# Kernel optimization log

Hardware: AMD Instinct MI355X
Metric: run time of the kernel (lower is better)

The kernel has to match this reference:

```python
import jax, jax.numpy as jnp
import numpy as np


def setup_inputs() -> dict:
    key = jax.random.key(0)
    ks = jax.random.split(key, 8)
    B, N, D = 8, 2048, 128
    s = 1.0 / float(np.sqrt(D))
    node = jax.random.normal(ks[0], (B, N, D), dtype=jnp.float32)
    node_mask = jax.random.randint(ks[1], (B, N), 0, 2, dtype=jnp.int32)
    punctuation_graph = jax.random.randint(ks[2], (B, N, N), 0, 2, dtype=jnp.int32)
    w_nw = jax.random.uniform(ks[3], (1, D), jnp.float32, -s, s)
    b_nw = jax.random.uniform(ks[4], (1,), jnp.float32, -s, s)
    w_self = jax.random.uniform(ks[5], (D, D), jnp.float32, -s, s)
    b_self = jax.random.uniform(ks[6], (D,), jnp.float32, -s, s)
    w_punct = jax.random.uniform(ks[7], (D, D), jnp.float32, -s, s)
    return {"node": node, "node_mask": node_mask, "punctuation_graph": punctuation_graph,
            "w_nw": w_nw, "b_nw": b_nw, "w_self": w_self, "b_self": b_self,
            "w_punct": w_punct, "iteration_steps": 2}


def reference(node, node_mask, punctuation_graph, w_nw, b_nw, w_self, b_self, w_punct, iteration_steps):
    B, N, D = node.shape
    # dd_graph = mask outer product with zeroed diagonal; graph = dd_graph * punctuation_graph
    eye = jnp.eye(N, dtype=punctuation_graph.dtype)
    dd = node_mask[:, None, :] * node_mask[:, :, None] * (1 - eye)[None, :, :]  # [B,N,N]
    graph = dd * punctuation_graph  # [B,N,N] int, binary
    nbr_num = graph.sum(-1)  # [B,N]
    # replace_masked_values(nbr_num, nbr_num>=1, 1): nodes with no neighbors get denom 1
    nbr_f = jnp.where(nbr_num >= 1, nbr_num.astype(node.dtype), jnp.asarray(1.0, node.dtype))
    gmask = graph > 0
    weights = []
    x = node
    for _ in range(iteration_steps):  # small fixed step count
        dw = jax.nn.sigmoid(jnp.einsum('bnd,od->bno', x, w_nw) + b_nw)[..., 0]  # [B,N]
        weights.append(dw)
        self_info = jnp.einsum('bnd,ed->bne', x, w_self) + b_self  # [B,N,D]
        info_p = jnp.einsum('bnd,ed->bne', x, w_punct)  # [B,N,D]
        # node_weight[b,i,j] = dw[b,j] where graph[b,i,j] else 0
        nw = jnp.where(gmask, dw[:, None, :], jnp.asarray(0.0, x.dtype))  # [B,N,N]
        agg = jnp.einsum('bnm,bmd->bnd', nw, info_p) / nbr_f[..., None]
        x = jax.nn.relu(self_info + agg)
    all_weight = jnp.stack(weights, axis=1)  # [B, steps, N]
    return x, all_weight
```

## Files before the change

kernel.cpp:

```cpp
#include <hip/hip_runtime.h>
#include <hip/hip_bf16.h>

#define BB 8
#define NN 2048
#define DD 128

typedef __attribute__((ext_vector_type(8))) __bf16 bf16x8;
typedef __attribute__((ext_vector_type(4))) float f32x4;
typedef __attribute__((ext_vector_type(4))) int   i32x4;

static __device__ __forceinline__ unsigned short f2bf(float f) {
    union { float f; unsigned u; } v; v.f = f;
    unsigned r = (v.u + 0x7FFFu + ((v.u >> 16) & 1u)) >> 16;
    return (unsigned short)r;
}
static __device__ __forceinline__ float bf2f(unsigned short b) {
    union { unsigned u; float f; } v; v.u = ((unsigned)b) << 16;
    return v.f;
}

__global__ __launch_bounds__(256) void kernPW(
    const int* __restrict__ punct, const int* __restrict__ mask,
    const float* __restrict__ node, const float* __restrict__ w_self,
    const float* __restrict__ w_punct,
    unsigned* __restrict__ pk, float* __restrict__ scale_g, float* __restrict__ pdm_g,
    unsigned short* __restrict__ xb, unsigned short* __restrict__ wsb,
    unsigned short* __restrict__ wpb)
{
    const int t = threadIdx.x;
    const int bid = blockIdx.x;

    if (bid < 4096) {
        const int wave = t >> 6, lane = t & 63;
        const int row_g = bid * 4 + wave;
        const int b = row_g >> 11;
        const int i = row_g & (NN - 1);

        const int* prow = punct + (size_t)row_g * NN;
        const int* mrow = mask + (size_t)b * NN;

        unsigned pk0 = 0, pk1 = 0;
        int acc = 0;
        #pragma unroll 4
        for (int w = 0; w < 32; ++w) {
            const int col = w * 64 + lane;
            const int p = prow[col];
            const int m = mrow[col];
            const int pred = (p & m) & 1;
            unsigned long long bal = __ballot(pred);
            if (lane == w) { pk0 = (unsigned)bal; pk1 = (unsigned)(bal >> 32); }
            acc += pred + ((col == i ? pred : 0) << 16);
        }
        #pragma unroll
        for (int o = 32; o > 0; o >>= 1) acc += __shfl_xor(acc, o, 64);

        if (lane < 32) {
            uint2 w2; w2.x = pk0; w2.y = pk1;
            *(uint2*)(pk + (size_t)row_g * 64 + 2 * lane) = w2;
        }
        if (lane == 0) {
            const int nall = acc & 0xFFFF;
            const int pdm  = acc >> 16;
            const int mi   = mrow[i];
            const int nbr  = nall - pdm;
            scale_g[row_g] = mi ? 1.f / (float)(nbr < 1 ? 1 : nbr) : 0.f;
            pdm_g[row_g]   = (float)pdm;
        }
        return;
    }

    const int cb = bid - 4096;
    const float* src; unsigned short* dst; size_t base;
    if (cb < 1024)      { src = node;    dst = xb;  base = (size_t)cb * 2048; }
    else if (cb < 1032) { src = w_self;  dst = wsb; base = (size_t)(cb - 1024) * 2048; }
    else                { src = w_punct; dst = wpb; base = (size_t)(cb - 1032) * 2048; }
    const size_t i0 = base + (size_t)t * 8;
    f32x4 a = *(const f32x4*)(src + i0);
    f32x4 c = *(const f32x4*)(src + i0 + 4);
    unsigned q0 = f2bf(a.x) | ((unsigned)f2bf(a.y) << 16);
    unsigned q1 = f2bf(a.z) | ((unsigned)f2bf(a.w) << 16);
    unsigned q2 = f2bf(c.x) | ((unsigned)f2bf(c.y) << 16);
    unsigned q3 = f2bf(c.z) | ((unsigned)f2bf(c.w) << 16);
    i32x4 pw = {(int)q0, (int)q1, (int)q2, (int)q3};
    *(i32x4*)(dst + i0) = pw;
}

__global__ __launch_bounds__(256) void kernB(
    const unsigned short* __restrict__ xb,
    const float* __restrict__ xf,
    const unsigned short* __restrict__ wsb,
    const unsigned short* __restrict__ wpb,
    const float* __restrict__ w_nw, const float* __restrict__ b_nw,
    const float* __restrict__ b_self,
    float* __restrict__ si_out,
    unsigned short* __restrict__ yne_out,
    unsigned short* __restrict__ yT_out,
    float* __restrict__ aw_out)
{
    __shared__ float dw_l[32];
    __shared__ unsigned short ytl[128 * 40];

    const int t  = threadIdx.x;
    const int n0 = blockIdx.x * 32;
    const int b  = n0 >> 11;
    const int nb = n0 & (NN - 1);
    const int wave = t >> 6, lane = t & 63;
    const int quad = lane >> 4, l16 = lane & 15;

    {
        const int row = wave * 8 + (lane >> 3);
        const int seg = (lane & 7) * 16;
        const float* xr = xf + (size_t)(n0 + row) * DD + seg;
        const float* wr = w_nw + seg;
        f32x4 a0 = *(const f32x4*)xr,       a1 = *(const f32x4*)(xr + 4);
        f32x4 a2 = *(const f32x4*)(xr + 8), a3 = *(const f32x4*)(xr + 12);
        f32x4 w0 = *(const f32x4*)wr,       w1 = *(const f32x4*)(wr + 4);
        f32x4 w2 = *(const f32x4*)(wr + 8), w3 = *(const f32x4*)(wr + 12);
        float s = a0.x*w0.x + a0.y*w0.y + a0.z*w0.z + a0.w*w0.w
                + a1.x*w1.x + a1.y*w1.y + a1.z*w1.z + a1.w*w1.w
                + a2.x*w2.x + a2.y*w2.y + a2.z*w2.z + a2.w*w2.w
                + a3.x*w3.x + a3.y*w3.y + a3.z*w3.z + a3.w*w3.w;
        s += __shfl_xor(s, 1, 64);
        s += __shfl_xor(s, 2, 64);
        s += __shfl_xor(s, 4, 64);
        if ((lane & 7) == 0) {
            float dv = 1.f / (1.f + __expf(-(s + b_nw[0])));
            dw_l[row] = dv;
            aw_out[(size_t)b * 2 * NN + nb + row] = dv;
        }
    }

    f32x4 accs[2][2] = {}, accp[2][2] = {};
    const unsigned short* xrow = xb + (size_t)n0 * DD;
    #pragma unroll
    for (int kk = 0; kk < 4; ++kk) {
        const int k0 = kk * 32 + quad * 8;
        bf16x8 af[2], bs[2], bp[2];
        #pragma unroll
        for (int mt = 0; mt < 2; ++mt)
            af[mt] = *(const bf16x8*)(xrow + (size_t)(mt * 16 + l16) * DD + k0);
        #pragma unroll
        for (int nt = 0; nt < 2; ++nt) {
            const int e = wave * 32 + nt * 16 + l16;
            bs[nt] = *(const bf16x8*)(wsb + (size_t)e * DD + k0);
            bp[nt] = *(const bf16x8*)(wpb + (size_t)e * DD + k0);
        }
        #pragma unroll
        for (int mt = 0; mt < 2; ++mt)
            #pragma unroll
            for (int nt = 0; nt < 2; ++nt) {
                accs[mt][nt] = __builtin_amdgcn_mfma_f32_16x16x32_bf16(af[mt], bs[nt], accs[mt][nt], 0, 0, 0);
                accp[mt][nt] = __builtin_amdgcn_mfma_f32_16x16x32_bf16(af[mt], bp[nt], accp[mt][nt], 0, 0, 0);
            }
    }

    __syncthreads();
    #pragma unroll
    for (int mt = 0; mt < 2; ++mt) {
        #pragma unroll
        for (int nt = 0; nt < 2; ++nt) {
            const int e = wave * 32 + nt * 16 + l16;
            const float bsv = b_self[e];
            #pragma unroll
            for (int r = 0; r < 4; ++r) {
                const int nl = mt * 16 + quad * 4 + r;
                const size_t idx = (size_t)(n0 + nl) * DD + e;
                si_out[idx] = accs[mt][nt][r] + bsv;
                const float yv = dw_l[nl] * accp[mt][nt][r];
                const unsigned short ub = f2bf(yv);
                yne_out[idx] = ub;
                ytl[e * 40 + nl] = ub;
            }
        }
    }
    __syncthreads();
    {
        const int e = t >> 1, half = t & 1;
        const i32x4* src = (const i32x4*)&ytl[e * 40 + half * 16];
        i32x4 v0 = src[0], v1 = src[1];
        i32x4* dst = (i32x4*)(yT_out + (size_t)(b * DD + e) * NN + nb + half * 16);
        dst[0] = v0; dst[1] = v1;
    }
}

__global__ __launch_bounds__(256) void kernC(
    const unsigned* __restrict__ pk,
    const float* __restrict__ scale_g, const float* __restrict__ pdm_g,
    const unsigned short* __restrict__ yT,
    const float* __restrict__ si,
    const unsigned short* __restrict__ yne,
    float* __restrict__ x_out,
    unsigned short* __restrict__ xb_out)
{
    __shared__ unsigned pPk[32 * 68];
    __shared__ float scale_l[32];
    __shared__ float pdm_l[32];

    const int t  = threadIdx.x;
    const int b  = blockIdx.x & 7;
    const int i0 = (blockIdx.x >> 3) * 32;
    const size_t rg0 = (size_t)b * NN + i0;

    #pragma unroll
    for (int r = 0; r < 2; ++r) {
        const int u   = r * 256 + t;
        const int row = u >> 4;
        const int wq  = (u & 15) * 4;
        i32x4 v = *(const i32x4*)(pk + (rg0 + row) * 64 + wq);
        *(i32x4*)&pPk[row * 68 + wq] = v;
    }
    if (t < 32) {
        scale_l[t] = scale_g[rg0 + t];
        pdm_l[t]   = pdm_g[rg0 + t];
    }
    __syncthreads();

    const int wn = t >> 6, lane = t & 63;
    const int quad = lane >> 4, l16 = lane & 15;
    const unsigned short* yTb = yT + (size_t)b * DD * NN;

    f32x4 acc[2][2] = {};

    #pragma unroll 4
    for (int kk = 0; kk < 64; ++kk) {
        bf16x8 bfr[2];
        #pragma unroll
        for (int nt = 0; nt < 2; ++nt) {
            const int e = wn * 32 + nt * 16 + l16;
            bfr[nt] = *(const bf16x8*)(yTb + (size_t)e * NN + kk * 32 + quad * 8);
        }
        bf16x8 af[2];
        #pragma unroll
        for (int mt = 0; mt < 2; ++mt) {
            const unsigned w = pPk[(mt * 16 + l16) * 68 + kk];
            const unsigned by = (w >> (quad * 8)) & 0xFFu;
            i32x4 ex;
            ex.x = ((by &   1u) ? 0x3F80 : 0) | ((by &   2u) ? 0x3F800000 : 0);
            ex.y = ((by &   4u) ? 0x3F80 : 0) | ((by &   8u) ? 0x3F800000 : 0);
            ex.z = ((by &  16u) ? 0x3F80 : 0) | ((by &  32u) ? 0x3F800000 : 0);
            ex.w = ((by &  64u) ? 0x3F80 : 0) | ((by & 128u) ? 0x3F800000 : 0);
            union { i32x4 i; bf16x8 h; } cv; cv.i = ex;
            af[mt] = cv.h;
        }
        #pragma unroll
        for (int mt = 0; mt < 2; ++mt)
            #pragma unroll
            for (int nt = 0; nt < 2; ++nt)
                acc[mt][nt] = __builtin_amdgcn_mfma_f32_16x16x32_bf16(af[mt], bfr[nt], acc[mt][nt], 0, 0, 0);
    }

    #pragma unroll
    for (int mt = 0; mt < 2; ++mt) {
        #pragma unroll
        for (int nt = 0; nt < 2; ++nt) {
            const int e = wn * 32 + nt * 16 + l16;
            #pragma unroll
            for (int r = 0; r < 4; ++r) {
                const int row = mt * 16 + quad * 4 + r;
                const size_t idx = (rg0 + row) * DD + e;
                const float yv = bf2f(yne[idx]);
                float v = si[idx] + scale_l[row] * (acc[mt][nt][r] - pdm_l[row] * yv);
                v = fmaxf(v, 0.f);
                x_out[idx]  = v;
                xb_out[idx] = f2bf(v);
            }
        }
    }
}

extern "C" void kernel_launch(void* const* d_in, const int* in_sizes, int n_in,
                              void* d_out, int out_size, void* d_ws, size_t ws_size,
                              hipStream_t stream) {
    const float* node   = (const float*)d_in[0];
    const int*   mask   = (const int*)  d_in[1];
    const int*   punct  = (const int*)  d_in[2];
    const float* w_nw   = (const float*)d_in[3];
    const float* b_nw   = (const float*)d_in[4];
    const float* w_self = (const float*)d_in[5];
    const float* b_self = (const float*)d_in[6];
    const float* w_punct= (const float*)d_in[7];

    float* xout = (float*)d_out;
    float* aw   = xout + (size_t)BB * NN * DD;

    char* w = (char*)d_ws;
    float*          si   = (float*)w;
    unsigned short* yne  = (unsigned short*)(w + (8u  << 20));
    unsigned short* yT   = (unsigned short*)(w + (12u << 20));
    unsigned*       pk   = (unsigned*)(w + (16u << 20));
    float*          scl  = (float*)(w + (20u << 20));
    float*          pdm  = (float*)(w + (20u << 20) + (64u << 10));
    unsigned short* xb   = (unsigned short*)(w + (21u << 20));
    unsigned short* wsb  = (unsigned short*)(w + (25u << 20));
    unsigned short* wpb  = (unsigned short*)(w + (25u << 20) + (32u << 10));

    dim3 blk(256);
    kernPW<<<dim3(5136), blk, 0, stream>>>(punct, mask, node, w_self, w_punct,
                                           pk, scl, pdm, xb, wsb, wpb);
    kernB<<<dim3(512), blk, 0, stream>>>(xb, node, wsb, wpb, w_nw, b_nw, b_self,
                                         si, yne, yT, aw);
    kernC<<<dim3(512), blk, 0, stream>>>(pk, scl, pdm, yT, si, yne, xout, xb);
    kernB<<<dim3(512), blk, 0, stream>>>(xb, xout, wsb, wpb, w_nw, b_nw, b_self,
                                         si, yne, yT, aw + NN);
    kernC<<<dim3(512), blk, 0, stream>>>(pk, scl, pdm, yT, si, yne, xout, xb);
}
```

Measured before the change: 304.3 us.

## Fuse both iteration steps into one persistent kernel with grid barrier

Replaces the four per-step launches with a single persistent kernel of 256 blocks of 512 threads. Each block keeps its weights, packed graph rows and 64-row activation tile in shared memory across both steps and synchronises the grid with an atomic-counter barrier. This removes launch gaps and the global round trips for self_info, y and the bf16 activations. The bf16 conversion of node and weights is folded into the kernel, and yT is double-buffered per step. The costs are lower parallelism (256 blocks), large shared memory use, and reliance on all blocks being co-resident for the spin barrier to avoid deadlock.

Result: slower. 347.1 us (+14.0%).

```diff
diff --git a/kernel.cpp b/kernel.cpp
--- a/kernel.cpp
+++ b/kernel.cpp
@@ -18,253 +18,287 @@
     union { unsigned u; float f; } v; v.u = ((unsigned)b) << 16;
     return v.f;
 }
-
-__global__ __launch_bounds__(256) void kernPW(
-    const int* __restrict__ punct, const int* __restrict__ mask,
-    const float* __restrict__ node, const float* __restrict__ w_self,
-    const float* __restrict__ w_punct,
-    unsigned* __restrict__ pk, float* __restrict__ scale_g, float* __restrict__ pdm_g,
-    unsigned short* __restrict__ xb, unsigned short* __restrict__ wsb,
-    unsigned short* __restrict__ wpb)
-{
-    const int t = threadIdx.x;
-    const int bid = blockIdx.x;
-
-    if (bid < 4096) {
-        const int wave = t >> 6, lane = t & 63;
-        const int row_g = bid * 4 + wave;
-        const int b = row_g >> 11;
-        const int i = row_g & (NN - 1);
-
-        const int* prow = punct + (size_t)row_g * NN;
-        const int* mrow = mask + (size_t)b * NN;
-
-        unsigned pk0 = 0, pk1 = 0;
-        int acc = 0;
-        #pragma unroll 4
-        for (int w = 0; w < 32; ++w) {
-            const int col = w * 64 + lane;
-            const int p = prow[col];
-            const int m = mrow[col];
-            const int pred = (p & m) & 1;
-            unsigned long long bal = __ballot(pred);
-            if (lane == w) { pk0 = (unsigned)bal; pk1 = (unsigned)(bal >> 32); }
-            acc += pred + ((col == i ? pred : 0) << 16);
-        }
-        #pragma unroll
-        for (int o = 32; o > 0; o >>= 1) acc += __shfl_xor(acc, o, 64);
-
-        if (lane < 32) {
-            uint2 w2; w2.x = pk0; w2.y = pk1;
-            *(uint2*)(pk + (size_t)row_g * 64 + 2 * lane) = w2;
-        }
-        if (lane == 0) {
-            const int nall = acc & 0xFFFF;
-            const int pdm  = acc >> 16;
-            const int mi   = mrow[i];
-            const int nbr  = nall - pdm;
-            scale_g[row_g] = mi ? 1.f / (float)(nbr < 1 ? 1 : nbr) : 0.f;
-            pdm_g[row_g]   = (float)pdm;
-        }
-        return;
-    }
-
-    const int cb = bid - 4096;
-    const float* src; unsigned short* dst; size_t base;
-    if (cb < 1024)      { src = node;    dst = xb;  base = (size_t)cb * 2048; }
-    else if (cb < 1032) { src = w_self;  dst = wsb; base = (size_t)(cb - 1024) * 2048; }
-    else                { src = w_punct; dst = wpb; base = (size_t)(cb - 1032) * 2048; }
-    const size_t i0 = base + (size_t)t * 8;
-    f32x4 a = *(const f32x4*)(src + i0);
-    f32x4 c = *(const f32x4*)(src + i0 + 4);
+static __device__ __forceinline__ i32x4 pack8(f32x4 a, f32x4 c) {
     unsigned q0 = f2bf(a.x) | ((unsigned)f2bf(a.y) << 16);
     unsigned q1 = f2bf(a.z) | ((unsigned)f2bf(a.w) << 16);
     unsigned q2 = f2bf(c.x) | ((unsigned)f2bf(c.y) << 16);
     unsigned q3 = f2bf(c.z) | ((unsigned)f2bf(c.w) << 16);
-    i32x4 pw = {(int)q0, (int)q1, (int)q2, (int)q3};
-    *(i32x4*)(dst + i0) = pw;
-}
-
-__global__ __launch_bounds__(256) void kernB(
-    const unsigned short* __restrict__ xb,
-    const float* __restrict__ xf,
-    const unsigned short* __restrict__ wsb,
-    const unsigned short* __restrict__ wpb,
+    i32x4 r = {(int)q0, (int)q1, (int)q2, (int)q3};
+    return r;
+}
+
+static __device__ __forceinline__ void gridBarrier(unsigned* cnt, unsigned target) {
+    __syncthreads();
+    if (threadIdx.x == 0) {
+        __threadfence();
+        atomicAdd(cnt, 1u);
+        while (__hip_atomic_load(cnt, __ATOMIC_ACQUIRE, __HIP_MEMORY_SCOPE_AGENT) < target) {
+            __builtin_amdgcn_s_sleep(2);
+        }
+    }
+    __syncthreads();
+}
+
+__global__ __launch_bounds__(256) void kernP(
+    const int* __restrict__ punct, const int* __restrict__ mask,
+    unsigned* __restrict__ pk, float* __restrict__ scale_g, float* __restrict__ pdm_g,
+    unsigned* __restrict__ cnt)
+{
+    if (blockIdx.x == 0 && threadIdx.x == 0) *cnt = 0u;
+
+    const int t = threadIdx.x;
+    const int wave = t >> 6, lane = t & 63;
+    const int row_g = blockIdx.x * 4 + wave;
+    const int b = row_g >> 11;
+    const int i = row_g & (NN - 1);
+
+    const int* prow = punct + (size_t)row_g * NN;
+    const int* mrow = mask + (size_t)b * NN;
+
+    unsigned pk0 = 0, pk1 = 0;
+    int acc = 0;
+    #pragma unroll 4
+    for (int w = 0; w < 32; ++w) {
+        const int col = w * 64 + lane;
+        const int p = prow[col];
+        const int m = mrow[col];
+        const int pred = (p & m) & 1;
+        unsigned long long bal = __ballot(pred);
+        if (lane == w) { pk0 = (unsigned)bal; pk1 = (unsigned)(bal >> 32); }
+        acc += pred + ((col == i ? pred : 0) << 16);
+    }
+    #pragma unroll
+    for (int o = 32; o > 0; o >>= 1) acc += __shfl_xor(acc, o, 64);
+
+    if (lane < 32) {
+        uint2 w2; w2.x = pk0; w2.y = pk1;
+        *(uint2*)(pk + (size_t)row_g * 64 + 2 * lane) = w2;
+    }
+    if (lane == 0) {
+        const int nall = acc & 0xFFFF;
+        const int pdm  = acc >> 16;
+        const int mi   = mrow[i];
+        const int nbr  = nall - pdm;
+        scale_g[row_g] = mi ? 1.f / (float)(nbr < 1 ? 1 : nbr) : 0.f;
+        pdm_g[row_g]   = (float)pdm;
+    }
+}
+
+#define SMEM_BYTES 152320
+
+__global__ __launch_bounds__(512) void kernF(
+    const float* __restrict__ node,
     const float* __restrict__ w_nw, const float* __restrict__ b_nw,
-    const float* __restrict__ b_self,
-    float* __restrict__ si_out,
-    unsigned short* __restrict__ yne_out,
-    unsigned short* __restrict__ yT_out,
-    float* __restrict__ aw_out)
-{
-    __shared__ float dw_l[32];
-    __shared__ unsigned short ytl[128 * 40];
-
-    const int t  = threadIdx.x;
-    const int n0 = blockIdx.x * 32;
-    const int b  = n0 >> 11;
-    const int nb = n0 & (NN - 1);
-    const int wave = t >> 6, lane = t & 63;
-    const int quad = lane >> 4, l16 = lane & 15;
-
-    {
-        const int row = wave * 8 + (lane >> 3);
-        const int seg = (lane & 7) * 16;
-        const float* xr = xf + (size_t)(n0 + row) * DD + seg;
-        const float* wr = w_nw + seg;
-        f32x4 a0 = *(const f32x4*)xr,       a1 = *(const f32x4*)(xr + 4);
-        f32x4 a2 = *(const f32x4*)(xr + 8), a3 = *(const f32x4*)(xr + 12);
-        f32x4 w0 = *(const f32x4*)wr,       w1 = *(const f32x4*)(wr + 4);
-        f32x4 w2 = *(const f32x4*)(wr + 8), w3 = *(const f32x4*)(wr + 12);
-        float s = a0.x*w0.x + a0.y*w0.y + a0.z*w0.z + a0.w*w0.w
-                + a1.x*w1.x + a1.y*w1.y + a1.z*w1.z + a1.w*w1.w
-                + a2.x*w2.x + a2.y*w2.y + a2.z*w2.z + a2.w*w2.w
-                + a3.x*w3.x + a3.y*w3.y + a3.z*w3.z + a3.w*w3.w;
-        s += __shfl_xor(s, 1, 64);
-        s += __shfl_xor(s, 2, 64);
-        s += __shfl_xor(s, 4, 64);
-        if ((lane & 7) == 0) {
-            float dv = 1.f / (1.f + __expf(-(s + b_nw[0])));
-            dw_l[row] = dv;
-            aw_out[(size_t)b * 2 * NN + nb + row] = dv;
-        }
-    }
-
-    f32x4 accs[2][2] = {}, accp[2][2] = {};
-    const unsigned short* xrow = xb + (size_t)n0 * DD;
-    #pragma unroll
-    for (int kk = 0; kk < 4; ++kk) {
-        const int k0 = kk * 32 + quad * 8;
-        bf16x8 af[2], bs[2], bp[2];
-        #pragma unroll
-        for (int mt = 0; mt < 2; ++mt)
-            af[mt] = *(const bf16x8*)(xrow + (size_t)(mt * 16 + l16) * DD + k0);
-        #pragma unroll
-        for (int nt = 0; nt < 2; ++nt) {
-            const int e = wave * 32 + nt * 16 + l16;
-            bs[nt] = *(const bf16x8*)(wsb + (size_t)e * DD + k0);
-            bp[nt] = *(const bf16x8*)(wpb + (size_t)e * DD + k0);
-        }
-        #pragma unroll
-        for (int mt = 0; mt < 2; ++mt)
-            #pragma unroll
-            for (int nt = 0; nt < 2; ++nt) {
-                accs[mt][nt] = __builtin_amdgcn_mfma_f32_16x16x32_bf16(af[mt], bs[nt], accs[mt][nt], 0, 0, 0);
-                accp[mt][nt] = __builtin_amdgcn_mfma_f32_16x16x32_bf16(af[mt], bp[nt], accp[mt][nt], 0, 0, 0);
-            }
-    }
-
-    __syncthreads();
-    #pragma unroll
-    for (int mt = 0; mt < 2; ++mt) {
-        #pragma unroll
-        for (int nt = 0; nt < 2; ++nt) {
-            const int e = wave * 32 + nt * 16 + l16;
-            const float bsv = b_self[e];
-            #pragma unroll
-            for (int r = 0; r < 4; ++r) {
-                const int nl = mt * 16 + quad * 4 + r;
-                const size_t idx = (size_t)(n0 + nl) * DD + e;
-                si_out[idx] = accs[mt][nt][r] + bsv;
-                const float yv = dw_l[nl] * accp[mt][nt][r];
-                const unsigned short ub = f2bf(yv);
-                yne_out[idx] = ub;
-                ytl[e * 40 + nl] = ub;
-            }
-        }
-    }
-    __syncthreads();
-    {
-        const int e = t >> 1, half = t & 1;
-        const i32x4* src = (const i32x4*)&ytl[e * 40 + half * 16];
-        i32x4 v0 = src[0], v1 = src[1];
-        i32x4* dst = (i32x4*)(yT_out + (size_t)(b * DD + e) * NN + nb + half * 16);
-        dst[0] = v0; dst[1] = v1;
-    }
-}
-
-__global__ __launch_bounds__(256) void kernC(
+    const float* __restrict__ w_self, const float* __restrict__ b_self,
+    const float* __restrict__ w_punct,
     const unsigned* __restrict__ pk,
     const float* __restrict__ scale_g, const float* __restrict__ pdm_g,
-    const unsigned short* __restrict__ yT,
-    const float* __restrict__ si,
-    const unsigned short* __restrict__ yne,
-    float* __restrict__ x_out,
-    unsigned short* __restrict__ xb_out)
+    unsigned short* __restrict__ yT0, unsigned short* __restrict__ yT1,
+    float* __restrict__ x_out, float* __restrict__ aw,
+    unsigned* __restrict__ cnt)
 {
-    __shared__ unsigned pPk[32 * 68];
-    __shared__ float scale_l[32];
-    __shared__ float pdm_l[32];
+    extern __shared__ char smem[];
+    unsigned short* wsL   = (unsigned short*)(smem);
+    unsigned short* wpL   = (unsigned short*)(smem + 32768);
+    unsigned*       pPk   = (unsigned*)(smem + 65536);
+    unsigned short* ytl   = (unsigned short*)(smem + 82944);
+    float*          xLf   = (float*)(smem + 101376);
+    unsigned short* xLb   = (unsigned short*)(smem + 134144);
+    float*          dw_l  = (float*)(smem + 150528);
+    float*          wnw_l = (float*)(smem + 150784);
+    float*          bself_l = (float*)(smem + 151296);
+    float*          scl_l = (float*)(smem + 151808);
+    float*          pdm_l = (float*)(smem + 152064);
 
     const int t  = threadIdx.x;
     const int b  = blockIdx.x & 7;
-    const int i0 = (blockIdx.x >> 3) * 32;
+    const int i0 = (blockIdx.x >> 3) * 64;
     const size_t rg0 = (size_t)b * NN + i0;
 
+    {
+        const int e = t >> 2, k0 = (t & 3) * 32;
+        const float* s1 = w_self  + (size_t)e * DD + k0;
+        const float* s2 = w_punct + (size_t)e * DD + k0;
+        #pragma unroll
+        for (int c = 0; c < 4; ++c) {
+            const int off = (e << 8) + (((k0 * 2) + (c << 4)) ^ ((e & 7) << 4));
+            f32x4 a = *(const f32x4*)(s1 + c * 8);
+            f32x4 d = *(const f32x4*)(s1 + c * 8 + 4);
+            *(i32x4*)((char*)wsL + off) = pack8(a, d);
+            f32x4 a2 = *(const f32x4*)(s2 + c * 8);
+            f32x4 d2 = *(const f32x4*)(s2 + c * 8 + 4);
+            *(i32x4*)((char*)wpL + off) = pack8(a2, d2);
+        }
+    }
     #pragma unroll
     for (int r = 0; r < 2; ++r) {
-        const int u   = r * 256 + t;
-        const int row = u >> 4;
-        const int wq  = (u & 15) * 4;
+        const int u = r * 512 + t;
+        const int row = u >> 4, wq = (u & 15) * 4;
         i32x4 v = *(const i32x4*)(pk + (rg0 + row) * 64 + wq);
         *(i32x4*)&pPk[row * 68 + wq] = v;
     }
-    if (t < 32) {
-        scale_l[t] = scale_g[rg0 + t];
-        pdm_l[t]   = pdm_g[rg0 + t];
-    }
+    if (t < 64)  { scl_l[t] = scale_g[rg0 + t]; pdm_l[t] = pdm_g[rg0 + t]; }
+    if (t < 128) { wnw_l[t] = w_nw[t]; bself_l[t] = b_self[t]; }
     __syncthreads();
 
-    const int wn = t >> 6, lane = t & 63;
+    const int wave = t >> 6, lane = t & 63;
+    const int wm = wave >> 2, wn = wave & 3;
     const int quad = lane >> 4, l16 = lane & 15;
-    const unsigned short* yTb = yT + (size_t)b * DD * NN;
-
-    f32x4 acc[2][2] = {};
-
-    #pragma unroll 4
-    for (int kk = 0; kk < 64; ++kk) {
-        bf16x8 bfr[2];
-        #pragma unroll
-        for (int nt = 0; nt < 2; ++nt) {
-            const int e = wn * 32 + nt * 16 + l16;
-            bfr[nt] = *(const bf16x8*)(yTb + (size_t)e * NN + kk * 32 + quad * 8);
-        }
-        bf16x8 af[2];
-        #pragma unroll
-        for (int mt = 0; mt < 2; ++mt) {
-            const unsigned w = pPk[(mt * 16 + l16) * 68 + kk];
-            const unsigned by = (w >> (quad * 8)) & 0xFFu;
-            i32x4 ex;
-            ex.x = ((by &   1u) ? 0x3F80 : 0) | ((by &   2u) ? 0x3F800000 : 0);
-            ex.y = ((by &   4u) ? 0x3F80 : 0) | ((by &   8u) ? 0x3F800000 : 0);
-            ex.z = ((by &  16u) ? 0x3F80 : 0) | ((by &  32u) ? 0x3F800000 : 0);
-            ex.w = ((by &  64u) ? 0x3F80 : 0) | ((by & 128u) ? 0x3F800000 : 0);
-            union { i32x4 i; bf16x8 h; } cv; cv.i = ex;
-            af[mt] = cv.h;
-        }
+    const float bnw0 = b_nw[0];
+
+    f32x4 accs[2][2];
+    f32x4 yv[2][2];
+
+    for (int step = 0; step < 2; ++step) {
+        unsigned short* yTs = step ? yT1 : yT0;
+
+        {
+            const int drow = wave * 8 + (lane >> 3);
+            const int dseg = (lane & 7) * 16;
+            const float* xr = step ? (xLf + drow * DD + dseg)
+                                   : (node + (rg0 + drow) * DD + dseg);
+            f32x4 a0 = *(const f32x4*)xr,        a1 = *(const f32x4*)(xr + 4);
+            f32x4 a2 = *(const f32x4*)(xr + 8),  a3 = *(const f32x4*)(xr + 12);
+            const float* wr = wnw_l + dseg;
+            float s = a0.x*wr[0]  + a0.y*wr[1]  + a0.z*wr[2]  + a0.w*wr[3]
+                    + a1.x*wr[4]  + a1.y*wr[5]  + a1.z*wr[6]  + a1.w*wr[7]
+                    + a2.x*wr[8]  + a2.y*wr[9]  + a2.z*wr[10] + a2.w*wr[11]
+                    + a3.x*wr[12] + a3.y*wr[13] + a3.z*wr[14] + a3.w*wr[15];
+            s += __shfl_xor(s, 1, 64);
+            s += __shfl_xor(s, 2, 64);
+            s += __shfl_xor(s, 4, 64);
+            if ((lane & 7) == 0) {
+                float dv = 1.f / (1.f + __expf(-(s + bnw0)));
+                dw_l[drow] = dv;
+                aw[((size_t)b * 2 + step) * NN + i0 + drow] = dv;
+            }
+        }
+
+        f32x4 accp[2][2];
         #pragma unroll
         for (int mt = 0; mt < 2; ++mt)
             #pragma unroll
+            for (int nt = 0; nt < 2; ++nt) {
+                accs[mt][nt] = (f32x4){0.f, 0.f, 0.f, 0.f};
+                accp[mt][nt] = (f32x4){0.f, 0.f, 0.f, 0.f};
+            }
+        #pragma unroll
+        for (int kk = 0; kk < 4; ++kk) {
+            const int k0 = kk * 32 + quad * 8;
+            bf16x8 af[2], bs[2], bp[2];
+            #pragma unroll
+            for (int mt = 0; mt < 2; ++mt) {
+                const int rl = wm * 32 + mt * 16 + l16;
+                if (step == 0) {
+                    const float* xs = node + (rg0 + rl) * DD + k0;
+                    f32x4 a = *(const f32x4*)xs, c = *(const f32x4*)(xs + 4);
+                    union { i32x4 i; bf16x8 h; } cv; cv.i = pack8(a, c);
+                    af[mt] = cv.h;
+                } else {
+                    const int off = (rl << 8) + ((k0 * 2) ^ ((rl & 7) << 4));
+                    af[mt] = *(const bf16x8*)((char*)xLb + off);
+                }
+            }
+            #pragma unroll
+            for (int nt = 0; nt < 2; ++nt) {
+                const int e = wn * 32 + nt * 16 + l16;
+                const int off = (e << 8) + ((k0 * 2) ^ ((e & 7) << 4));
+                bs[nt] = *(const bf16x8*)((char*)wsL + off);
+                bp[nt] = *(const bf16x8*)((char*)wpL + off);
+            }
+            #pragma unroll
+            for (int mt = 0; mt < 2; ++mt)
+                #pragma unroll
+                for (int nt = 0; nt < 2; ++nt) {
+                    accs[mt][nt] = __builtin_amdgcn_mfma_f32_16x16x32_bf16(af[mt], bs[nt], accs[mt][nt], 0, 0, 0);
+                    accp[mt][nt] = __builtin_amdgcn_mfma_f32_16x16x32_bf16(af[mt], bp[nt], accp[mt][nt], 0, 0, 0);
+                }
+        }
+        __syncthreads();
+
+        #pragma unroll
+        for (int mt = 0; mt < 2; ++mt)
+            #pragma unroll
+            for (int nt = 0; nt < 2; ++nt) {
+                const int e = wn * 32 + nt * 16 + l16;
+                const float bsv = bself_l[e];
+                #pragma unroll
+                for (int r = 0; r < 4; ++r) {
+                    const int rl = wm * 32 + mt * 16 + quad * 4 + r;
+                    accs[mt][nt][r] += bsv;
+                    const float yval = dw_l[rl] * accp[mt][nt][r];
+                    const unsigned short ub = f2bf(yval);
+                    yv[mt][nt][r] = bf2f(ub);
+                    ytl[e * 72 + rl] = ub;
+                }
+            }
+        __syncthreads();
+        {
+            const int e2 = t >> 2, qh = t & 3;
+            const i32x4* src = (const i32x4*)&ytl[e2 * 72 + qh * 16];
+            i32x4 v0 = src[0], v1 = src[1];
+            i32x4* dst = (i32x4*)(yTs + (size_t)(b * DD + e2) * NN + i0 + qh * 16);
+            dst[0] = v0; dst[1] = v1;
+        }
+
+        gridBarrier(cnt, 256u * (unsigned)(step + 1));
+
+        f32x4 acc[2][2];
+        #pragma unroll
+        for (int mt = 0; mt < 2; ++mt)
+            #pragma unroll
             for (int nt = 0; nt < 2; ++nt)
-                acc[mt][nt] = __builtin_amdgcn_mfma_f32_16x16x32_bf16(af[mt], bfr[nt], acc[mt][nt], 0, 0, 0);
-    }
-
-    #pragma unroll
-    for (int mt = 0; mt < 2; ++mt) {
-        #pragma unroll
-        for (int nt = 0; nt < 2; ++nt) {
-            const int e = wn * 32 + nt * 16 + l16;
-            #pragma unroll
-            for (int r = 0; r < 4; ++r) {
-                const int row = mt * 16 + quad * 4 + r;
-                const size_t idx = (rg0 + row) * DD + e;
-                const float yv = bf2f(yne[idx]);
-                float v = si[idx] + scale_l[row] * (acc[mt][nt][r] - pdm_l[row] * yv);
-                v = fmaxf(v, 0.f);
-                x_out[idx]  = v;
-                xb_out[idx] = f2bf(v);
-            }
-        }
+                acc[mt][nt] = (f32x4){0.f, 0.f, 0.f, 0.f};
+
+        const unsigned short* yTb = yTs + (size_t)b * DD * NN;
+        #pragma unroll 4
+        for (int kk = 0; kk < 64; ++kk) {
+            bf16x8 bfr[2];
+            #pragma unroll
+            for (int nt = 0; nt < 2; ++nt) {
+                const int e = wn * 32 + nt * 16 + l16;
+                bfr[nt] = *(const bf16x8*)(yTb + (size_t)e * NN + kk * 32 + quad * 8);
+            }
+            bf16x8 af[2];
+            #pragma unroll
+            for (int mt = 0; mt < 2; ++mt) {
+                const unsigned w = pPk[(wm * 32 + mt * 16 + l16) * 68 + kk];
+                const unsigned by = (w >> (quad * 8)) & 0xFFu;
+                i32x4 ex;
+                ex.x = ((by &   1u) ? 0x3F80 : 0) | ((by &   2u) ? 0x3F800000 : 0);
+                ex.y = ((by &   4u) ? 0x3F80 : 0) | ((by &   8u) ? 0x3F800000 : 0);
+                ex.z = ((by &  16u) ? 0x3F80 : 0) | ((by &  32u) ? 0x3F800000 : 0);
+                ex.w = ((by &  64u) ? 0x3F80 : 0) | ((by & 128u) ? 0x3F800000 : 0);
+                union { i32x4 i; bf16x8 h; } cv; cv.i = ex;
+                af[mt] = cv.h;
+            }
+            #pragma unroll
+            for (int mt = 0; mt < 2; ++mt)
+                #pragma unroll
+                for (int nt = 0; nt < 2; ++nt)
+                    acc[mt][nt] = __builtin_amdgcn_mfma_f32_16x16x32_bf16(af[mt], bfr[nt], acc[mt][nt], 0, 0, 0);
+        }
+
+        #pragma unroll
+        for (int mt = 0; mt < 2; ++mt)
+            #pragma unroll
+            for (int nt = 0; nt < 2; ++nt) {
+                const int e = wn * 32 + nt * 16 + l16;
+                #pragma unroll
+                for (int r = 0; r < 4; ++r) {
+                    const int rl = wm * 32 + mt * 16 + quad * 4 + r;
+                    float v = accs[mt][nt][r] + scl_l[rl] * (acc[mt][nt][r] - pdm_l[rl] * yv[mt][nt][r]);
+                    v = fmaxf(v, 0.f);
+                    if (step == 0) {
+                        xLf[rl * DD + e] = v;
+                        const int off = (rl << 8) + ((e * 2) ^ ((rl & 7) << 4));
+                        *(unsigned short*)((char*)xLb + off) = f2bf(v);
+                    } else {
+                        x_out[(rg0 + rl) * DD + e] = v;
+                    }
+                }
+            }
+        if (step == 0) __syncthreads();
     }
 }
 
@@ -284,23 +318,22 @@
     float* aw   = xout + (size_t)BB * NN * DD;
 
     char* w = (char*)d_ws;
-    float*          si   = (float*)w;
-    unsigned short* yne  = (unsigned short*)(w + (8u  << 20));
-    unsigned short* yT   = (unsigned short*)(w + (12u << 20));
-    unsigned*       pk   = (unsigned*)(w + (16u << 20));
-    float*          scl  = (float*)(w + (20u << 20));
-    float*          pdm  = (float*)(w + (20u << 20) + (64u << 10));
-    unsigned short* xb   = (unsigned short*)(w + (21u << 20));
-    unsigned short* wsb  = (unsigned short*)(w + (25u << 20));
-    unsigned short* wpb  = (unsigned short*)(w + (25u << 20) + (32u << 10));
-
-    dim3 blk(256);
-    kernPW<<<dim3(5136), blk, 0, stream>>>(punct, mask, node, w_self, w_punct,
-                                           pk, scl, pdm, xb, wsb, wpb);
-    kernB<<<dim3(512), blk, 0, stream>>>(xb, node, wsb, wpb, w_nw, b_nw, b_self,
-                                         si, yne, yT, aw);
-    kernC<<<dim3(512), blk, 0, stream>>>(pk, scl, pdm, yT, si, yne, xout, xb);
-    kernB<<<dim3(512), blk, 0, stream>>>(xb, xout, wsb, wpb, w_nw, b_nw, b_self,
-                                         si, yne, yT, aw + NN);
-    kernC<<<dim3(512), blk, 0, stream>>>(pk, scl, pdm, yT, si, yne, xout, xb);
-}
+    unsigned short* yT0 = (unsigned short*)w;
+    unsigned short* yT1 = (unsigned short*)(w + (4u << 20));
+    unsigned*       pk  = (unsigned*)(w + (8u << 20));
+    float*          scl = (float*)(w + (12u << 20));
+    float*          pdm = (float*)(w + (12u << 20) + (64u << 10));
+    unsigned*       cnt = (unsigned*)(w + (12u << 20) + (128u << 10));
+
+    static bool attrSet = false;
+    if (!attrSet) {
+        hipFuncSetAttribute(reinterpret_cast<const void*>(kernF),
+                            hipFuncAttributeMaxDynamicSharedMemorySize, SMEM_BYTES);
+        attrSet = true;
+    }
+
+    kernP<<<dim3(4096), dim3(256), 0, stream>>>(punct, mask, pk, scl, pdm, cnt);
+    kernF<<<dim3(256), dim3(512), SMEM_BYTES, stream>>>(
+        node, w_nw, b_nw, w_self, b_self, w_punct,
+        pk, scl, pdm, yT0, yT1, xout, aw, cnt);
+}
```
